# Performance work log

Measured on AMD Instinct MI355X. Metric: run time of the kernel, lower is better.

## Reference

```python
import jax, jax.numpy as jnp
import numpy as np

B, L_ENC, L_DEC, D = 16, 512, 128, 1024


def setup_inputs() -> dict:
    key = jax.random.key(0)
    k1, k2, k3, k4, k5, k6 = jax.random.split(key, 6)
    encoder_hc = jax.random.normal(k1, (B, L_ENC, D), dtype=jnp.float32)
    decoder_hq = jax.random.normal(k2, (B, L_DEC, D), dtype=jnp.float32)
    # linear_sim: Linear(3*D, 1) -> weight vector [3D] + scalar bias
    w_sim = jax.random.normal(k3, (3 * D,), dtype=jnp.float32) * 0.02
    b_sim = jax.random.normal(k4, (1,), dtype=jnp.float32) * 0.02
    # linear_QV: Linear(4*D, D); stored as [4D, D] so y = x @ W_qv + b_qv
    W_qv = jax.random.normal(k5, (4 * D, D), dtype=jnp.float32) * 0.02
    b_qv = jax.random.normal(k6, (D,), dtype=jnp.float32) * 0.02
    return {"encoder_hc": encoder_hc, "decoder_hq": decoder_hq,
            "w_sim": w_sim, "b_sim": b_sim, "W_qv": W_qv, "b_qv": b_qv}


def reference(encoder_hc, decoder_hq, w_sim, b_sim, W_qv, b_qv):
    d = encoder_hc.shape[-1]
    w1, w2, w3 = w_sim[:d], w_sim[d:2 * d], w_sim[2 * d:]
    # Fused trilinear similarity: Sim[b,i,j] = w1.hc_i + w2.hq_j + w3.(hc_i*hq_j) + b
    # (algebraically identical to linear_sim(cat[hc_i, hq_j, hc_i*hq_j]))
    Sim = ((encoder_hc @ w1)[:, :, None]            # [B, L_enc, 1]
           + (decoder_hq @ w2)[:, None, :]          # [B, 1, L_dec]
           + jnp.einsum('bid,bjd->bij', encoder_hc * w3, decoder_hq)
           + b_sim[0])                              # [B, L_enc, L_dec]
    # Context-to-query attention
    A = jax.nn.softmax(Sim, axis=2)
    hq_hat = jnp.einsum('bij,bjd->bid', A, decoder_hq)          # [B, L_enc, D]
    # Query-to-context attention (max over decoder positions)
    Batt = jax.nn.softmax(jnp.max(Sim, axis=2), axis=1)          # [B, L_enc]
    hc_bar = jnp.einsum('bi,bid->bd', Batt, encoder_hc)[:, None, :]  # [B, 1, D]
    hc_hat = jnp.broadcast_to(hc_bar, encoder_hc.shape)          # tiled over L_enc
    feats = jnp.concatenate(
        [encoder_hc, hq_hat, encoder_hc * hq_hat, encoder_hc * hc_hat], axis=-1)
    hcq = feats @ W_qv + b_qv                                    # [B, L_enc, D]
    return hcq
```

## Files before the change

### kernel.cpp

```cpp
#include <hip/hip_runtime.h>

#define DEV __device__ __forceinline__

typedef __bf16 bf16;
typedef __bf16 bf16x4 __attribute__((ext_vector_type(4)));
typedef __bf16 bf16x8 __attribute__((ext_vector_type(8)));
typedef float f32x4 __attribute__((ext_vector_type(4)));

constexpr int BB = 16, LE = 512, LD = 128, DD = 1024;
constexpr int MALL = BB * LE;
constexpr int K4 = 4 * DD;

constexpr size_t OFF_FEATS = 0;
constexpr size_t OFF_HQW3  = OFF_FEATS + (size_t)MALL * K4 * 2;
constexpr size_t OFF_HQT   = OFF_HQW3 + (size_t)BB * LD * DD * 2;
constexpr size_t OFF_WT    = OFF_HQT + (size_t)BB * DD * LD * 2;
constexpr size_t OFF_ABF   = OFF_WT + (size_t)K4 * DD * 2;
constexpr size_t OFF_S1    = OFF_ABF + (size_t)MALL * LD * 2;
constexpr size_t OFF_S2    = OFF_S1 + (size_t)MALL * 4;
constexpr size_t OFF_MROW  = OFF_S2 + (size_t)BB * LD * 4;
constexpr size_t OFF_HCBAR = OFF_MROW + (size_t)MALL * 4;

DEV void gload16(const void* g, void* l) {
  __builtin_amdgcn_global_load_lds(
      (const __attribute__((address_space(1))) void*)g,
      (__attribute__((address_space(3))) void*)l, 16, 0, 0);
}

__global__ __launch_bounds__(256) void k_prep(const float* __restrict__ hc,
                                              const float* __restrict__ hq,
                                              const float* __restrict__ wsim,
                                              bf16* __restrict__ feats,
                                              bf16* __restrict__ hqw3,
                                              float* __restrict__ s1,
                                              float* __restrict__ s2) {
  const int r = blockIdx.x;
  const int t = threadIdx.x;
  __shared__ float red[4];
  float dot;
  if (r < MALL) {
    const float4 v = reinterpret_cast<const float4*>(hc + (size_t)r * DD)[t];
    const float4 w = reinterpret_cast<const float4*>(wsim)[t];
    bf16x4 o; o[0] = (bf16)v.x; o[1] = (bf16)v.y; o[2] = (bf16)v.z; o[3] = (bf16)v.w;
    *reinterpret_cast<bf16x4*>(feats + (size_t)r * K4 + t * 4) = o;
    dot = v.x * w.x + v.y * w.y + v.z * w.z + v.w * w.w;
  } else {
    const int rw = r - MALL;
    const float4 v = reinterpret_cast<const float4*>(hq + (size_t)rw * DD)[t];
    const float4 w2 = reinterpret_cast<const float4*>(wsim + DD)[t];
    const float4 w3 = reinterpret_cast<const float4*>(wsim + 2 * DD)[t];
    bf16x4 o; o[0] = (bf16)(v.x * w3.x); o[1] = (bf16)(v.y * w3.y);
    o[2] = (bf16)(v.z * w3.z); o[3] = (bf16)(v.w * w3.w);
    *reinterpret_cast<bf16x4*>(hqw3 + (size_t)rw * DD + t * 4) = o;
    dot = v.x * w2.x + v.y * w2.y + v.z * w2.z + v.w * w2.w;
  }
  #pragma unroll
  for (int o = 32; o; o >>= 1) dot += __shfl_down(dot, o);
  const int lane = t & 63, w = t >> 6;
  if (lane == 0) red[w] = dot;
  __syncthreads();
  if (t == 0) {
    float s = red[0] + red[1] + red[2] + red[3];
    if (r < MALL) s1[r] = s; else s2[r - MALL] = s;
  }
}

__global__ __launch_bounds__(256) void k_transpose(const float* __restrict__ in,
                                                   bf16* __restrict__ out,
                                                   int R, int C, long ibs, long obs) {
  __shared__ float tile[64][68];
  const float* inp = in + (size_t)blockIdx.z * ibs;
  bf16* outp = out + (size_t)blockIdx.z * obs;
  const int r0 = blockIdx.y * 64, c0 = blockIdx.x * 64;
  const int t = threadIdx.x;
  #pragma unroll
  for (int i = 0; i < 4; i++) {
    const int r = i * 16 + (t >> 4), c = (t & 15) << 2;
    const float4 v = *reinterpret_cast<const float4*>(inp + (size_t)(r0 + r) * C + c0 + c);
    tile[r][c] = v.x; tile[r][c + 1] = v.y; tile[r][c + 2] = v.z; tile[r][c + 3] = v.w;
  }
  __syncthreads();
  {
    const int oc = t >> 2;
    const int g = t & 3;
    bf16x8 t0, t1;
    #pragma unroll
    for (int i = 0; i < 8; i++) t0[i] = (bf16)tile[g * 16 + i][oc];
    #pragma unroll
    for (int i = 0; i < 8; i++) t1[i] = (bf16)tile[g * 16 + 8 + i][oc];
    bf16* op = outp + (size_t)(c0 + oc) * R + r0 + g * 16;
    *reinterpret_cast<bf16x8*>(op) = t0;
    *reinterpret_cast<bf16x8*>(op + 8) = t1;
  }
}

template <int KTILES>
DEV void gemm_core(char* smem,
                   const bf16* __restrict__ Ag, int lda,
                   const bf16* __restrict__ Bg, int ldb,
                   f32x4 acc[4][4]) {
  bf16* As = (bf16*)smem;
  bf16* Bs = (bf16*)(smem + 16384);
  const int t = threadIdx.x;
  const int lane = t & 63;
  const int w = t >> 6;
  const int wm = w >> 1, wn = w & 1;
  const int l8 = lane >> 3, lc = lane & 7;
  const int ar = lane & 15;
  const int ak = (lane >> 4) * 8;
  const f32x4 zero = {0.f, 0.f, 0.f, 0.f};
  #pragma unroll
  for (int i = 0; i < 4; i++)
    #pragma unroll
    for (int j = 0; j < 4; j++) acc[i][j] = zero;

  for (int kt = 0; kt < KTILES; kt++) {
    const int k0 = kt * 64;
    #pragma unroll
    for (int c = 0; c < 4; c++) {
      const int row = c * 32 + w * 8 + l8;
      gload16(Ag + (size_t)row * lda + k0 + lc * 8, (char*)As + c * 4096 + w * 1024);
      gload16(Bg + (size_t)row * ldb + k0 + lc * 8, (char*)Bs + c * 4096 + w * 1024);
    }
    __syncthreads();
    #pragma unroll
    for (int kk = 0; kk < 2; kk++) {
      bf16x8 a[4], b[4];
      #pragma unroll
      for (int i = 0; i < 4; i++) {
        a[i] = *reinterpret_cast<const bf16x8*>(&As[(wm * 64 + i * 16 + ar) * 64 + kk * 32 + ak]);
        b[i] = *reinterpret_cast<const bf16x8*>(&Bs[(wn * 64 + i * 16 + ar) * 64 + kk * 32 + ak]);
      }
      #pragma unroll
      for (int i = 0; i < 4; i++)
        #pragma unroll
        for (int j = 0; j < 4; j++)
          acc[i][j] = __builtin_amdgcn_mfma_f32_16x16x32_bf16(a[i], b[j], acc[i][j], 0, 0, 0);
    }
    __syncthreads();
  }
}

__global__ __launch_bounds__(256) void k_sim(const bf16* __restrict__ feats,
                                             const bf16* __restrict__ hqw3,
                                             const float* __restrict__ s1,
                                             const float* __restrict__ s2,
                                             const float* __restrict__ bsim,
                                             bf16* __restrict__ Abf,
                                             float* __restrict__ mrow) {
  __shared__ __align__(16) char smem[128 * 129 * 4];
  __shared__ float invs[128];
  const int b = blockIdx.x, it = blockIdx.y;
  const int m0 = b * LE + it * 128;
  const int t = threadIdx.x;
  f32x4 acc[4][4];
  gemm_core<16>(smem, feats + (size_t)m0 * K4, K4, hqw3 + (size_t)b * LD * DD, DD, acc);

  float* simt = (float*)smem;
  const float bs = bsim[0];
  const int lane = t & 63, w = t >> 6, wm = w >> 1, wn = w & 1;
  #pragma unroll
  for (int i = 0; i < 4; i++)
    #pragma unroll
    for (int r = 0; r < 4; r++) {
      const int ml = wm * 64 + i * 16 + (lane >> 4) * 4 + r;
      const float s1v = s1[m0 + ml] + bs;
      #pragma unroll
      for (int j = 0; j < 4; j++) {
        const int nl = wn * 64 + j * 16 + (lane & 15);
        simt[ml * 129 + nl] = acc[i][j][r] + s1v + s2[b * LD + nl];
      }
    }
  __syncthreads();

  {
    const int row = t >> 1, half = t & 1;
    float* rp = simt + row * 129 + half * 64;
    float m = rp[0];
    #pragma unroll
    for (int k = 1; k < 64; k++) m = fmaxf(m, rp[k]);
    m = fmaxf(m, __shfl_xor(m, 1));
    float s = 0.f;
    #pragma unroll
    for (int k = 0; k < 64; k++) { const float e = __expf(rp[k] - m); rp[k] = e; s += e; }
    s += __shfl_xor(s, 1);
    if (half == 0) { invs[row] = 1.0f / s; mrow[m0 + row] = m; }
  }
  __syncthreads();

  #pragma unroll
  for (int it8 = 0; it8 < 8; it8++) {
    const int rr = it8 * 16 + (t >> 4), cc = (t & 15) * 8;
    const float iv = invs[rr];
    bf16x8 o;
    #pragma unroll
    for (int u = 0; u < 8; u++) o[u] = (bf16)(simt[rr * 129 + cc + u] * iv);
    *reinterpret_cast<bf16x8*>(Abf + (size_t)(m0 + rr) * LD + cc) = o;
  }
}

__global__ __launch_bounds__(256) void k_batt(const float* __restrict__ mrow,
                                              const float* __restrict__ hc,
                                              float* __restrict__ hcbar) {
  const int b = blockIdx.x, dc = blockIdx.y, t = threadIdx.x;
  __shared__ float batt[512];
  __shared__ float red[4];
  const int lane = t & 63, w = t >> 6;
  const float m0 = mrow[b * LE + t], m1 = mrow[b * LE + 256 + t];
  float m = fmaxf(m0, m1);
  #pragma unroll
  for (int o = 32; o; o >>= 1) m = fmaxf(m, __shfl_xor(m, o));
  if (lane == 0) red[w] = m;
  __syncthreads();
  m = fmaxf(fmaxf(red[0], red[1]), fmaxf(red[2], red[3]));
  const float e0 = __expf(m0 - m), e1 = __expf(m1 - m);
  float s = e0 + e1;
  #pragma unroll
  for (int o = 32; o; o >>= 1) s += __shfl_xor(s, o);
  __syncthreads();
  if (lane == 0) red[w] = s;
  __syncthreads();
  s = red[0] + red[1] + red[2] + red[3];
  const float inv = 1.0f / s;
  batt[t] = e0 * inv;
  batt[t + 256] = e1 * inv;
  __syncthreads();
  const int d = dc * 256 + t;
  float acc = 0.0f;
  const float* hcb = hc + (size_t)b * LE * DD + d;
  #pragma unroll 8
  for (int i = 0; i < LE; i++) acc += batt[i] * hcb[(size_t)i * DD];
  hcbar[b * DD + d] = acc;
}

__global__ __launch_bounds__(256) void k_hqhat(const bf16* __restrict__ Abf,
                                               const bf16* __restrict__ hqT,
                                               const float* __restrict__ hc,
                                               const float* __restrict__ hcbar,
                                               bf16* __restrict__ feats) {
  __shared__ __align__(16) char smem[128 * 136 * 2];
  const int b = blockIdx.x, it = blockIdx.y, nt = blockIdx.z;
  const int m0 = b * LE + it * 128;
  const int n0 = nt * 128;
  const int t = threadIdx.x;
  f32x4 acc[4][4];
  gemm_core<2>(smem, Abf + (size_t)m0 * LD, LD,
               hqT + (size_t)b * DD * LD + (size_t)n0 * LD, LD, acc);

  bf16* tile = (bf16*)smem;
  const int lane = t & 63, w = t >> 6, wm = w >> 1, wn = w & 1;
  #pragma unroll
  for (int i = 0; i < 4; i++)
    #pragma unroll
    for (int j = 0; j < 4; j++)
      #pragma unroll
      for (int r = 0; r < 4; r++) {
        const int ml = wm * 64 + i * 16 + (lane >> 4) * 4 + r;
        const int nl = wn * 64 + j * 16 + (lane & 15);
        tile[ml * 136 + nl] = (bf16)acc[i][j][r];
      }
  __syncthreads();

  const int d = n0 + (t & 15) * 8;
  const float4 hb0 = *reinterpret_cast<const float4*>(hcbar + b * DD + d);
  const float4 hb1 = *reinterpret_cast<const float4*>(hcbar + b * DD + d + 4);
  const float hbv[8] = {hb0.x, hb0.y, hb0.z, hb0.w, hb1.x, hb1.y, hb1.z, hb1.w};
  #pragma unroll
  for (int it8 = 0; it8 < 8; it8++) {
    const int rr = it8 * 16 + (t >> 4);
    const int m = m0 + rr;
    const bf16x8 hv = *reinterpret_cast<const bf16x8*>(&tile[rr * 136 + (t & 15) * 8]);
    const float4 c0 = *reinterpret_cast<const float4*>(hc + (size_t)m * DD + d);
    const float4 c1 = *reinterpret_cast<const float4*>(hc + (size_t)m * DD + d + 4);
    const float hcv[8] = {c0.x, c0.y, c0.z, c0.w, c1.x, c1.y, c1.z, c1.w};
    bf16x8 q2, q3;
    #pragma unroll
    for (int u = 0; u < 8; u++) {
      q2[u] = (bf16)(hcv[u] * (float)hv[u]);
      q3[u] = (bf16)(hcv[u] * hbv[u]);
    }
    bf16* f = feats + (size_t)m * K4;
    *reinterpret_cast<bf16x8*>(f + DD + d) = hv;
    *reinterpret_cast<bf16x8*>(f + 2 * DD + d) = q2;
    *reinterpret_cast<bf16x8*>(f + 3 * DD + d) = q3;
  }
}

__global__ __launch_bounds__(512, 2) void k_final2(const bf16* __restrict__ feats,
                                                   const bf16* __restrict__ WT,
                                                   const float* __restrict__ bqv,
                                                   float* __restrict__ out) {
  __shared__ __align__(16) char smem[3 * 49152];
  const int mt = blockIdx.x, nt = blockIdx.y;
  const int t = threadIdx.x;
  const int lane = t & 63, w = t >> 6;
  const int wm = w >> 1, wn = w & 1;
  const int l8 = lane >> 3, lc = lane & 7;
  const int ar = lane & 15;
  const int cg = lane >> 4;
  const int a7 = lane & 7;
  const int arow = w * 8 + l8;
  const int schunk = (lc ^ l8) * 8;
  const int w8 = w * 8;

  const bf16* Ag = feats + (size_t)mt * 256 * K4;
  const bf16* Bg = WT + (size_t)nt * 128 * K4;

  f32x4 acc[4][4];
  const f32x4 zero = {0.f, 0.f, 0.f, 0.f};
  #pragma unroll
  for (int i = 0; i < 4; i++)
    #pragma unroll
    for (int j = 0; j < 4; j++) acc[i][j] = zero;

  #define STAGE_A(base, c, k0) \
    gload16(Ag + (size_t)((c) * 64 + arow) * K4 + (k0) + schunk, (base) + ((c) * 64 + w8) * 128)
  #define STAGE_B(base, c, k0) \
    gload16(Bg + (size_t)((c) * 64 + arow) * K4 + (k0) + schunk, (base) + 32768 + ((c) * 64 + w8) * 128)

  #define LDA(base, i, kk) \
    (*(const bf16x8*)((base) + (wm * 64 + (i) * 16 + ar) * 128 + (((kk) * 4 + cg) ^ a7) * 16))
  #define LDB(base, j, kk) \
    (*(const bf16x8*)((base) + 32768 + (wn * 64 + (j) * 16 + ar) * 128 + (((kk) * 4 + cg) ^ a7) * 16))

  {
    char* b0 = smem;
    STAGE_A(b0, 0, 0); STAGE_A(b0, 1, 0); STAGE_A(b0, 2, 0); STAGE_A(b0, 3, 0);
    STAGE_B(b0, 0, 0); STAGE_B(b0, 1, 0);
    char* b1 = smem + 49152;
    STAGE_A(b1, 0, 64); STAGE_A(b1, 1, 64); STAGE_A(b1, 2, 64); STAGE_A(b1, 3, 64);
    STAGE_B(b1, 0, 64); STAGE_B(b1, 1, 64);
  }
  asm volatile("s_waitcnt vmcnt(6)" ::: "memory");
  __builtin_amdgcn_s_barrier();

  int rd = 0, st = 2;
  for (int kt = 0; kt < 64; kt++) {
    char* bA = smem + rd * 49152;
    char* sA = smem + st * 49152;
    const int k2 = (kt + 2) * 64;
    const bool do_stage = (kt + 2) < 64;
    bf16x8 a0[4], b0[4], a1[4], b1[4];

    #pragma unroll
    for (int i = 0; i < 4; i++) a0[i] = LDA(bA, i, 0);
    #pragma unroll
    for (int j = 0; j < 4; j++) b0[j] = LDB(bA, j, 0);
    #pragma unroll
    for (int i = 0; i < 4; i++) a1[i] = LDA(bA, i, 1);
    #pragma unroll
    for (int j = 0; j < 4; j++) b1[j] = LDB(bA, j, 1);
    if (do_stage) {
      STAGE_A(sA, 0, k2); STAGE_A(sA, 1, k2); STAGE_A(sA, 2, k2); STAGE_A(sA, 3, k2);
      STAGE_B(sA, 0, k2); STAGE_B(sA, 1, k2);
    }

    __builtin_amdgcn_s_setprio(1);
    #pragma unroll
    for (int i = 0; i < 4; i++)
      #pragma unroll
      for (int j = 0; j < 4; j++)
        acc[i][j] = __builtin_amdgcn_mfma_f32_16x16x32_bf16(a0[i], b0[j], acc[i][j], 0, 0, 0);
    #pragma unroll
    for (int i = 0; i < 4; i++)
      #pragma unroll
      for (int j = 0; j < 4; j++)
        acc[i][j] = __builtin_amdgcn_mfma_f32_16x16x32_bf16(a1[i], b1[j], acc[i][j], 0, 0, 0);
    __builtin_amdgcn_s_setprio(0);

    if (do_stage) asm volatile("s_waitcnt vmcnt(6)" ::: "memory");
    else          asm volatile("s_waitcnt vmcnt(0)" ::: "memory");
    __builtin_amdgcn_s_barrier();

    rd = (rd == 2) ? 0 : rd + 1;
    st = (st == 2) ? 0 : st + 1;
  }
  #undef STAGE_A
  #undef STAGE_B
  #undef LDA
  #undef LDB

  __builtin_amdgcn_sched_barrier(0);

  float* tile = (float*)smem;
  const int cc = (t & 31) * 4;
  const float4 bq = *reinterpret_cast<const float4*>(bqv + nt * 128 + cc);
  __syncthreads();
  #pragma unroll
  for (int p = 0; p < 4; p++) {
    if (wm == p) {
      #pragma unroll
      for (int i = 0; i < 4; i++)
        #pragma unroll
        for (int j = 0; j < 4; j++)
          #pragma unroll
          for (int r = 0; r < 4; r++) {
            const int ml = i * 16 + (lane >> 4) * 4 + r;
            const int nl = wn * 64 + j * 16 + (lane & 15);
            tile[ml * 132 + nl] = acc[i][j][r];
          }
    }
    __syncthreads();
    #pragma unroll
    for (int itx = 0; itx < 4; itx++) {
      const int rr = itx * 16 + (t >> 5);
      const f32x4 v = *reinterpret_cast<const f32x4*>(&tile[rr * 132 + cc]);
      float4 o;
      o.x = v[0] + bq.x; o.y = v[1] + bq.y; o.z = v[2] + bq.z; o.w = v[3] + bq.w;
      *reinterpret_cast<float4*>(out + (size_t)(mt * 256 + p * 64 + rr) * DD + nt * 128 + cc) = o;
    }
    __syncthreads();
  }
}

extern "C" void kernel_launch(void* const* d_in, const int* in_sizes, int n_in,
                              void* d_out, int out_size, void* d_ws, size_t ws_size,
                              hipStream_t stream) {
  const float* hc = (const float*)d_in[0];
  const float* hq = (const float*)d_in[1];
  const float* wsim = (const float*)d_in[2];
  const float* bsim = (const float*)d_in[3];
  const float* Wqv = (const float*)d_in[4];
  const float* bqv = (const float*)d_in[5];
  float* out = (float*)d_out;

  char* ws = (char*)d_ws;
  bf16* feats = (bf16*)(ws + OFF_FEATS);
  bf16* hqw3 = (bf16*)(ws + OFF_HQW3);
  bf16* hqT = (bf16*)(ws + OFF_HQT);
  bf16* WT = (bf16*)(ws + OFF_WT);
  bf16* Abf = (bf16*)(ws + OFF_ABF);
  float* s1 = (float*)(ws + OFF_S1);
  float* s2 = (float*)(ws + OFF_S2);
  float* mrow = (float*)(ws + OFF_MROW);
  float* hcbar = (float*)(ws + OFF_HCBAR);

  k_prep<<<MALL + BB * LD, 256, 0, stream>>>(hc, hq, wsim, feats, hqw3, s1, s2);
  k_transpose<<<dim3(DD / 64, LD / 64, BB), 256, 0, stream>>>(hq, hqT, LD, DD,
                                                              (long)LD * DD, (long)DD * LD);
  k_transpose<<<dim3(DD / 64, K4 / 64, 1), 256, 0, stream>>>(Wqv, WT, K4, DD, 0, 0);
  k_sim<<<dim3(BB, LE / 128), 256, 0, stream>>>(feats, hqw3, s1, s2, bsim, Abf, mrow);
  k_batt<<<dim3(BB, DD / 256), 256, 0, stream>>>(mrow, hc, hcbar);
  k_hqhat<<<dim3(BB, LE / 128, DD / 128), 256, 0, stream>>>(Abf, hqT, hc, hcbar, feats);
  k_final2<<<dim3(MALL / 256, DD / 128), 512, 0, stream>>>(feats, WT, bqv, out);
}
```

Baseline: 243.0 us.

## Merge prep and transpose kernels; halve GEMM K-tile to raise occupancy

After: 245.3 us. Within noise of the previous version (+1.0%).

```diff
diff --git a/kernel.cpp b/kernel.cpp
--- a/kernel.cpp
+++ b/kernel.cpp
@@ -27,52 +27,67 @@
       (__attribute__((address_space(3))) void*)l, 16, 0, 0);
 }
 
-__global__ __launch_bounds__(256) void k_prep(const float* __restrict__ hc,
-                                              const float* __restrict__ hq,
-                                              const float* __restrict__ wsim,
-                                              bf16* __restrict__ feats,
-                                              bf16* __restrict__ hqw3,
-                                              float* __restrict__ s1,
-                                              float* __restrict__ s2) {
-  const int r = blockIdx.x;
+constexpr int NPREP = MALL + BB * LD;
+constexpr int NTHQ  = NPREP + (DD / 64) * (LD / 64) * BB;
+constexpr int NTW   = NTHQ + (DD / 64) * (K4 / 64);
+
+__global__ __launch_bounds__(256) void k_pre(const float* __restrict__ hc,
+                                             const float* __restrict__ hq,
+                                             const float* __restrict__ wsim,
+                                             const float* __restrict__ Wqv,
+                                             bf16* __restrict__ feats,
+                                             bf16* __restrict__ hqw3,
+                                             bf16* __restrict__ hqT,
+                                             bf16* __restrict__ WT,
+                                             float* __restrict__ s1,
+                                             float* __restrict__ s2) {
+  __shared__ __align__(16) float tile[64][68];
+  const int bid = blockIdx.x;
   const int t = threadIdx.x;
-  __shared__ float red[4];
-  float dot;
-  if (r < MALL) {
-    const float4 v = reinterpret_cast<const float4*>(hc + (size_t)r * DD)[t];
-    const float4 w = reinterpret_cast<const float4*>(wsim)[t];
-    bf16x4 o; o[0] = (bf16)v.x; o[1] = (bf16)v.y; o[2] = (bf16)v.z; o[3] = (bf16)v.w;
-    *reinterpret_cast<bf16x4*>(feats + (size_t)r * K4 + t * 4) = o;
-    dot = v.x * w.x + v.y * w.y + v.z * w.z + v.w * w.w;
+
+  if (bid < NPREP) {
+    const int r = bid;
+    float dot;
+    if (r < MALL) {
+      const float4 v = reinterpret_cast<const float4*>(hc + (size_t)r * DD)[t];
+      const float4 w = reinterpret_cast<const float4*>(wsim)[t];
+      bf16x4 o; o[0] = (bf16)v.x; o[1] = (bf16)v.y; o[2] = (bf16)v.z; o[3] = (bf16)v.w;
+      *reinterpret_cast<bf16x4*>(feats + (size_t)r * K4 + t * 4) = o;
+      dot = v.x * w.x + v.y * w.y + v.z * w.z + v.w * w.w;
+    } else {
+      const int rw = r - MALL;
+      const float4 v = reinterpret_cast<const float4*>(hq + (size_t)rw * DD)[t];
+      const float4 w2 = reinterpret_cast<const float4*>(wsim + DD)[t];
+      const float4 w3 = reinterpret_cast<const float4*>(wsim + 2 * DD)[t];
+      bf16x4 o; o[0] = (bf16)(v.x * w3.x); o[1] = (bf16)(v.y * w3.y);
+      o[2] = (bf16)(v.z * w3.z); o[3] = (bf16)(v.w * w3.w);
+      *reinterpret_cast<bf16x4*>(hqw3 + (size_t)rw * DD + t * 4) = o;
+      dot = v.x * w2.x + v.y * w2.y + v.z * w2.z + v.w * w2.w;
+    }
+    #pragma unroll
+    for (int o = 32; o; o >>= 1) dot += __shfl_down(dot, o);
+    const int lane = t & 63, w = t >> 6;
+    float* red = &tile[0][0];
+    if (lane == 0) red[w] = dot;
+    __syncthreads();
+    if (t == 0) {
+      float s = red[0] + red[1] + red[2] + red[3];
+      if (r < MALL) s1[r] = s; else s2[r - MALL] = s;
+    }
+    return;
+  }
+
+  const float* inp; bf16* outp; int R, C, r0, c0;
+  if (bid < NTHQ) {
+    const int b2 = bid - NPREP;
+    const int x = b2 & 15, y = (b2 >> 4) & 1, z = b2 >> 5;
+    inp = hq + (size_t)z * LD * DD; outp = hqT + (size_t)z * DD * LD;
+    R = LD; C = DD; r0 = y * 64; c0 = x * 64;
   } else {
-    const int rw = r - MALL;
-    const float4 v = reinterpret_cast<const float4*>(hq + (size_t)rw * DD)[t];
-    const float4 w2 = reinterpret_cast<const float4*>(wsim + DD)[t];
-    const float4 w3 = reinterpret_cast<const float4*>(wsim + 2 * DD)[t];
-    bf16x4 o; o[0] = (bf16)(v.x * w3.x); o[1] = (bf16)(v.y * w3.y);
-    o[2] = (bf16)(v.z * w3.z); o[3] = (bf16)(v.w * w3.w);
-    *reinterpret_cast<bf16x4*>(hqw3 + (size_t)rw * DD + t * 4) = o;
-    dot = v.x * w2.x + v.y * w2.y + v.z * w2.z + v.w * w2.w;
-  }
-  #pragma unroll
-  for (int o = 32; o; o >>= 1) dot += __shfl_down(dot, o);
-  const int lane = t & 63, w = t >> 6;
-  if (lane == 0) red[w] = dot;
-  __syncthreads();
-  if (t == 0) {
-    float s = red[0] + red[1] + red[2] + red[3];
-    if (r < MALL) s1[r] = s; else s2[r - MALL] = s;
-  }
-}
-
-__global__ __launch_bounds__(256) void k_transpose(const float* __restrict__ in,
-                                                   bf16* __restrict__ out,
-                                                   int R, int C, long ibs, long obs) {
-  __shared__ float tile[64][68];
-  const float* inp = in + (size_t)blockIdx.z * ibs;
-  bf16* outp = out + (size_t)blockIdx.z * obs;
-  const int r0 = blockIdx.y * 64, c0 = blockIdx.x * 64;
-  const int t = threadIdx.x;
+    const int b2 = bid - NTHQ;
+    const int x = b2 & 15, y = b2 >> 4;
+    inp = Wqv; outp = WT; R = K4; C = DD; r0 = y * 64; c0 = x * 64;
+  }
   #pragma unroll
   for (int i = 0; i < 4; i++) {
     const int r = i * 16 + (t >> 4), c = (t & 15) << 2;
@@ -286,22 +301,20 @@
   }
 }
 
-__global__ __launch_bounds__(512, 2) void k_final2(const bf16* __restrict__ feats,
+__global__ __launch_bounds__(512, 4) void k_final3(const bf16* __restrict__ feats,
                                                    const bf16* __restrict__ WT,
                                                    const float* __restrict__ bqv,
                                                    float* __restrict__ out) {
-  __shared__ __align__(16) char smem[3 * 49152];
+  __shared__ __align__(16) char smem[3 * 24576];
   const int mt = blockIdx.x, nt = blockIdx.y;
   const int t = threadIdx.x;
   const int lane = t & 63, w = t >> 6;
   const int wm = w >> 1, wn = w & 1;
-  const int l8 = lane >> 3, lc = lane & 7;
   const int ar = lane & 15;
   const int cg = lane >> 4;
-  const int a7 = lane & 7;
-  const int arow = w * 8 + l8;
-  const int schunk = (lc ^ l8) * 8;
-  const int w8 = w * 8;
+  const int srow = w * 16 + (lane >> 2);
+  const int schunk = (lane & 3) * 8;
+  const int wbase = w * 1024;
 
   const bf16* Ag = feats + (size_t)mt * 256 * K4;
   const bf16* Bg = WT + (size_t)nt * 128 * K4;
@@ -313,72 +326,55 @@
     #pragma unroll
     for (int j = 0; j < 4; j++) acc[i][j] = zero;
 
-  #define STAGE_A(base, c, k0) \
-    gload16(Ag + (size_t)((c) * 64 + arow) * K4 + (k0) + schunk, (base) + ((c) * 64 + w8) * 128)
-  #define STAGE_B(base, c, k0) \
-    gload16(Bg + (size_t)((c) * 64 + arow) * K4 + (k0) + schunk, (base) + 32768 + ((c) * 64 + w8) * 128)
-
-  #define LDA(base, i, kk) \
-    (*(const bf16x8*)((base) + (wm * 64 + (i) * 16 + ar) * 128 + (((kk) * 4 + cg) ^ a7) * 16))
-  #define LDB(base, j, kk) \
-    (*(const bf16x8*)((base) + 32768 + (wn * 64 + (j) * 16 + ar) * 128 + (((kk) * 4 + cg) ^ a7) * 16))
+  #define STAGE_A3(base, c, k0) \
+    gload16(Ag + (size_t)((c) * 128 + srow) * K4 + (k0) + schunk, (base) + (c) * 8192 + wbase)
+  #define STAGE_B3(base, k0) \
+    gload16(Bg + (size_t)srow * K4 + (k0) + schunk, (base) + 16384 + wbase)
+  #define LDA3(base, i) (*(const bf16x8*)((base) + (wm * 64 + (i) * 16 + ar) * 64 + cg * 16))
+  #define LDB3(base, j) (*(const bf16x8*)((base) + 16384 + (wn * 64 + (j) * 16 + ar) * 64 + cg * 16))
 
   {
     char* b0 = smem;
-    STAGE_A(b0, 0, 0); STAGE_A(b0, 1, 0); STAGE_A(b0, 2, 0); STAGE_A(b0, 3, 0);
-    STAGE_B(b0, 0, 0); STAGE_B(b0, 1, 0);
-    char* b1 = smem + 49152;
-    STAGE_A(b1, 0, 64); STAGE_A(b1, 1, 64); STAGE_A(b1, 2, 64); STAGE_A(b1, 3, 64);
-    STAGE_B(b1, 0, 64); STAGE_B(b1, 1, 64);
-  }
-  asm volatile("s_waitcnt vmcnt(6)" ::: "memory");
+    STAGE_A3(b0, 0, 0); STAGE_A3(b0, 1, 0); STAGE_B3(b0, 0);
+    char* b1 = smem + 24576;
+    STAGE_A3(b1, 0, 32); STAGE_A3(b1, 1, 32); STAGE_B3(b1, 32);
+  }
+  asm volatile("s_waitcnt vmcnt(3)" ::: "memory");
   __builtin_amdgcn_s_barrier();
 
   int rd = 0, st = 2;
-  for (int kt = 0; kt < 64; kt++) {
-    char* bA = smem + rd * 49152;
-    char* sA = smem + st * 49152;
-    const int k2 = (kt + 2) * 64;
-    const bool do_stage = (kt + 2) < 64;
-    bf16x8 a0[4], b0[4], a1[4], b1[4];
-
-    #pragma unroll
-    for (int i = 0; i < 4; i++) a0[i] = LDA(bA, i, 0);
-    #pragma unroll
-    for (int j = 0; j < 4; j++) b0[j] = LDB(bA, j, 0);
-    #pragma unroll
-    for (int i = 0; i < 4; i++) a1[i] = LDA(bA, i, 1);
-    #pragma unroll
-    for (int j = 0; j < 4; j++) b1[j] = LDB(bA, j, 1);
-    if (do_stage) {
-      STAGE_A(sA, 0, k2); STAGE_A(sA, 1, k2); STAGE_A(sA, 2, k2); STAGE_A(sA, 3, k2);
-      STAGE_B(sA, 0, k2); STAGE_B(sA, 1, k2);
-    }
+  for (int kt = 0; kt < 128; kt++) {
+    char* bA = smem + rd * 24576;
+    char* sA = smem + st * 24576;
+    const int k2 = (kt + 2) * 32;
+    const bool do_stage = (kt + 2) < 128;
+    bf16x8 a[4], b[4];
+
+    #pragma unroll
+    for (int i = 0; i < 4; i++) a[i] = LDA3(bA, i);
+    #pragma unroll
+    for (int j = 0; j < 4; j++) b[j] = LDB3(bA, j);
+    if (do_stage) { STAGE_A3(sA, 0, k2); STAGE_A3(sA, 1, k2); STAGE_B3(sA, k2); }
 
     __builtin_amdgcn_s_setprio(1);
     #pragma unroll
     for (int i = 0; i < 4; i++)
       #pragma unroll
       for (int j = 0; j < 4; j++)
-        acc[i][j] = __builtin_amdgcn_mfma_f32_16x16x32_bf16(a0[i], b0[j], acc[i][j], 0, 0, 0);
-    #pragma unroll
-    for (int i = 0; i < 4; i++)
-      #pragma unroll
-      for (int j = 0; j < 4; j++)
-        acc[i][j] = __builtin_amdgcn_mfma_f32_16x16x32_bf16(a1[i], b1[j], acc[i][j], 0, 0, 0);
+        acc[i][j] = __builtin_amdgcn_mfma_f32_16x16x32_bf16(a[i], b[j], acc[i][j], 0, 0, 0);
     __builtin_amdgcn_s_setprio(0);
 
-    if (do_stage) asm volatile("s_waitcnt vmcnt(6)" ::: "memory");
+    if (do_stage) asm volatile("s_waitcnt vmcnt(3)" ::: "memory");
     else          asm volatile("s_waitcnt vmcnt(0)" ::: "memory");
     __builtin_amdgcn_s_barrier();
 
     rd = (rd == 2) ? 0 : rd + 1;
     st = (st == 2) ? 0 : st + 1;
   }
-  #undef STAGE_A
-  #undef STAGE_B
-  #undef LDA
-  #undef LDB
+  #undef STAGE_A3
+  #undef STAGE_B3
+  #undef LDA3
+  #undef LDB3
 
   __builtin_amdgcn_sched_barrier(0);
 
@@ -435,12 +431,9 @@
   float* mrow = (float*)(ws + OFF_MROW);
   float* hcbar = (float*)(ws + OFF_HCBAR);
 
-  k_prep<<<MALL + BB * LD, 256, 0, stream>>>(hc, hq, wsim, feats, hqw3, s1, s2);
-  k_transpose<<<dim3(DD / 64, LD / 64, BB), 256, 0, stream>>>(hq, hqT, LD, DD,
-                                                              (long)LD * DD, (long)DD * LD);
-  k_transpose<<<dim3(DD / 64, K4 / 64, 1), 256, 0, stream>>>(Wqv, WT, K4, DD, 0, 0);
+  k_pre<<<NTW, 256, 0, stream>>>(hc, hq, wsim, Wqv, feats, hqw3, hqT, WT, s1, s2);
   k_sim<<<dim3(BB, LE / 128), 256, 0, stream>>>(feats, hqw3, s1, s2, bsim, Abf, mrow);
   k_batt<<<dim3(BB, DD / 256), 256, 0, stream>>>(mrow, hc, hcbar);
   k_hqhat<<<dim3(BB, LE / 128, DD / 128), 256, 0, stream>>>(Abf, hqT, hc, hcbar, feats);
-  k_final2<<<dim3(MALL / 256, DD / 128), 512, 0, stream>>>(feats, WT, bqv, out);
-}
+  k_final3<<<dim3(MALL / 256, DD / 128), 512, 0, stream>>>(feats, WT, bqv, out);
+}
```
